# Kernel optimization log

Hardware: AMD Instinct MI355X
Metric: run time of the kernel (lower is better)

The kernel has to match this reference:

```python
import jax, jax.numpy as jnp
import numpy as np

NB, NLOC, DIN, DOUT = 4, 4096, 512, 512
NTYPES, TEBD = 128, 128
N_EXPERTS, TOP_K = 8, 2  # share_expert = 0 -> routed_experts = 8, routed_top_k = 2


def setup_inputs() -> dict:
    key = jax.random.key(0)
    k = jax.random.split(key, 6)
    return {
        "x": jax.random.normal(k[0], (NB, NLOC, DIN), dtype=jnp.float32),
        "type_embeddings": jax.random.normal(k[1], (NTYPES, TEBD), dtype=jnp.float32),
        "atom_types": jax.random.randint(k[2], (NB, NLOC), 0, NTYPES, dtype=jnp.int32),
        "Wg": jax.random.normal(k[3], (TEBD, N_EXPERTS), dtype=jnp.float32) / np.sqrt(TEBD),
        "We": jax.random.normal(k[4], (N_EXPERTS, DIN, DOUT), dtype=jnp.float32) / np.sqrt(DIN),
        "be": jax.random.normal(k[5], (N_EXPERTS, DOUT), dtype=jnp.float32) * 0.01,
    }


def reference(x, type_embeddings, atom_types, Wg, We, be):
    # --- route: gate on type embeddings, then index per atom (MD-continuous) ---
    logits = type_embeddings @ Wg                       # [ntypes, E]
    top_vals, top_idx = jax.lax.top_k(logits, TOP_K)    # [ntypes, K]
    weights = jax.nn.softmax(top_vals, axis=-1)         # softmax over selected logits
    atom_w = weights[atom_types]                        # [nb, nloc, K]
    atom_i = top_idx[atom_types]                        # [nb, nloc, K]

    # scatter-add top-k weights into dense per-expert weights (matches scatter_add_)
    onehot = jax.nn.one_hot(atom_i, N_EXPERTS, dtype=x.dtype)   # [nb, nloc, K, E]
    per_expert_w = jnp.einsum("bnk,bnke->bne", atom_w, onehot)  # [nb, nloc, E]

    # --- run all experts densely (the batched JIT-friendly path), then combine ---
    expert_out = jnp.tanh(jnp.einsum("bnd,edo->bneo", x, We) + be)  # [nb, nloc, E, dout]
    out = jnp.einsum("bne,bneo->bno", per_expert_w, expert_out)     # [nb, nloc, dout]
    return out
```

## Files before the change

### kernel.cpp

```cpp
#include <hip/hip_runtime.h>
#include <hip/hip_bf16.h>
#include <math.h>

typedef __bf16 bf16;
typedef __bf16 bf16x8 __attribute__((ext_vector_type(8)));
typedef float  f32x4  __attribute__((ext_vector_type(4)));

#define NTOK   16384
#define DIN    512
#define DOUT   512
#define NTYPES 128
#define TEBD   128
#define NEXP   8
#define NPAIR  64
#define MAXTILE 192

#define WS_ROUTE_P 0
#define WS_ROUTE_W 1024
#define WS_CNT     3072
#define WS_OFF     3584
#define WS_BASE    4096
#define WS_NTILE   4608
#define WS_TMAP    5120
#define WS_RMAP    8192
#define WS_WGT     (WS_RMAP + NTOK * 4)
#define WS_XG      (WS_WGT + NTOK * 8)
#define WS_WET     (WS_XG + (size_t)NTOK * DIN * 2)

#define GLOAD_LDS16(g, l)                                                     \
  __builtin_amdgcn_global_load_lds(                                           \
      (const __attribute__((address_space(1))) void*)(g),                     \
      (__attribute__((address_space(3))) void*)(l), 16, 0, 0)

__global__ void route_kernel(const float* __restrict__ emb,
                             const float* __restrict__ Wg,
                             int* __restrict__ route_p,
                             float* __restrict__ route_w,
                             int* __restrict__ cnt,
                             int* __restrict__ off) {
  int t = threadIdx.x;
  if (t < NPAIR) { cnt[t] = 0; off[t] = 0; }
  if (t >= NTYPES) return;
  const float* er = emb + (size_t)t * TEBD;
  float lg[NEXP];
#pragma unroll
  for (int e = 0; e < NEXP; ++e) lg[e] = 0.f;
  for (int j = 0; j < TEBD; ++j) {
    float ev = er[j];
#pragma unroll
    for (int e = 0; e < NEXP; ++e) lg[e] += ev * Wg[j * NEXP + e];
  }
  float v0 = -__builtin_inff(), v1 = -__builtin_inff();
  int i0 = 0, i1 = 0;
#pragma unroll
  for (int e = 0; e < NEXP; ++e) {
    float v = lg[e];
    if (v > v0) { v1 = v0; i1 = i0; v0 = v; i0 = e; }
    else if (v > v1) { v1 = v; i1 = e; }
  }
  float d = expf(v1 - v0);
  float inv = 1.f / (1.f + d);
  route_p[t] = i0 * 8 + i1;
  route_w[t * 2 + 0] = inv;
  route_w[t * 2 + 1] = d * inv;
}

__global__ void count_kernel(const int* __restrict__ atype,
                             const int* __restrict__ route_p,
                             int* __restrict__ cnt) {
  __shared__ int lc[NPAIR];
  int tid = threadIdx.x;
  if (tid < NPAIR) lc[tid] = 0;
  __syncthreads();
  int t = blockIdx.x * 256 + tid;
  int p = route_p[atype[t]];
  atomicAdd(&lc[p], 1);
  __syncthreads();
  if (tid < NPAIR && lc[tid]) atomicAdd(&cnt[tid], lc[tid]);
}

__global__ void scan_kernel(const int* __restrict__ cnt,
                            int* __restrict__ base,
                            int* __restrict__ ntile,
                            int* __restrict__ tmap) {
  __shared__ int sb[NPAIR];
  __shared__ int st[NPAIR];
  int l = threadIdx.x;
  int c = cnt[l];
  sb[l] = c;
  st[l] = (c + 127) >> 7;
  __syncthreads();
  int b = 0, tb = 0;
  for (int j = 0; j < l; ++j) { b += sb[j]; tb += st[j]; }
  base[l] = b;
  int nt_l = st[l];
  for (int i = 0; i < nt_l; ++i) {
    tmap[(tb + i) * 2 + 0] = l;
    tmap[(tb + i) * 2 + 1] = i * 128;
  }
  if (l == NPAIR - 1) ntile[0] = tb + nt_l;
}

__global__ void place_kernel(const int* __restrict__ atype,
                             const int* __restrict__ route_p,
                             const float* __restrict__ route_w,
                             const int* __restrict__ base,
                             int* __restrict__ off,
                             int* __restrict__ row_map,
                             float* __restrict__ wgt) {
  __shared__ int lc[NPAIR];
  __shared__ int lb[NPAIR];
  int tid = threadIdx.x;
  if (tid < NPAIR) lc[tid] = 0;
  __syncthreads();
  int t = blockIdx.x * 256 + tid;
  int ty = atype[t];
  int p = route_p[ty];
  int r = atomicAdd(&lc[p], 1);
  __syncthreads();
  if (tid < NPAIR) lb[tid] = lc[tid] ? atomicAdd(&off[tid], lc[tid]) : 0;
  __syncthreads();
  int pos = base[p] + lb[p] + r;
  row_map[pos] = t;
  ((float2*)wgt)[pos] = ((const float2*)route_w)[ty];
}

__global__ void gather_cvt_kernel(const float* __restrict__ x,
                                  const int* __restrict__ row_map,
                                  bf16* __restrict__ xg) {
  int gid = blockIdx.x * 256 + threadIdx.x;
  int row = gid >> 6;
  int c8 = (gid & 63) * 8;
  int tok = row_map[row];
  const float4* p = (const float4*)(x + (size_t)tok * DIN + c8);
  float4 a = p[0], b = p[1];
  bf16x8 o;
  o[0] = (bf16)a.x; o[1] = (bf16)a.y; o[2] = (bf16)a.z; o[3] = (bf16)a.w;
  o[4] = (bf16)b.x; o[5] = (bf16)b.y; o[6] = (bf16)b.z; o[7] = (bf16)b.w;
  *(bf16x8*)(xg + (size_t)row * DIN + c8) = o;
}

__global__ void cvt_weT_kernel(const float* __restrict__ We, bf16* __restrict__ WeT) {
  __shared__ float t[64][65];
  int bx = blockIdx.x;
  int e = bx >> 6;
  int rem = bx & 63;
  int kt = (rem >> 3) * 64;
  int nt = (rem & 7) * 64;
  int tid = threadIdx.x;
  int col = tid & 63;
  int rq = tid >> 6;
#pragma unroll
  for (int r = 0; r < 16; ++r) {
    int row = rq * 16 + r;
    t[row][col] = We[((size_t)e * DIN + kt + row) * DOUT + nt + col];
  }
  __syncthreads();
#pragma unroll
  for (int r = 0; r < 16; ++r) {
    int n = rq * 16 + r;
    WeT[((size_t)e * DOUT + nt + n) * DIN + kt + col] = (bf16)t[col][n];
  }
}

__global__ __launch_bounds__(256, 3) void moe_gemm_pair_kernel(
    const bf16* __restrict__ xg, const bf16* __restrict__ WeT,
    const float* __restrict__ be, const int* __restrict__ cnt,
    const int* __restrict__ base, const int* __restrict__ ntile,
    const int* __restrict__ tmap, const int* __restrict__ row_map,
    const float* __restrict__ wgt, float* __restrict__ out) {
  int nwork = ntile[0] * 8;
  int f = blockIdx.y * 8 + blockIdx.x;
  if (f >= nwork) return;
  int q = nwork >> 3, r = nwork & 7;
  int xcd = f & 7, idx = f >> 3;
  int L = (xcd < r ? xcd * (q + 1) : r * (q + 1) + (xcd - r) * q) + idx;
  int ti = L >> 3;
  int cx = L & 7;
  int list = tmap[ti * 2 + 0];
  int r0   = tmap[ti * 2 + 1];
  int e0 = list >> 3, e1 = list & 7;
  int nrow = cnt[list] - r0;
  if (nrow > 128) nrow = 128;
  int c0 = cx * 64;
  int arow0 = base[list] + r0;

  __shared__ __align__(16) bf16 As[3][128 * 32];
  __shared__ __align__(16) bf16 B0s[3][64 * 32];
  __shared__ __align__(16) bf16 B1s[3][64 * 32];
  __shared__ int   tokS[128];
  __shared__ float w0S[128], w1S[128];
  __shared__ float be0S[64], be1S[64];

  int tid = threadIdx.x;
  int lane = tid & 63, w = tid >> 6;

  if (tid < 128) {
    int srow = (tid < nrow) ? tid : (nrow - 1);
    int gl = arow0 + srow;
    tokS[tid] = row_map[gl];
    float2 ww = ((const float2*)wgt)[gl];
    w0S[tid] = ww.x;
    w1S[tid] = ww.y;
    if (tid < 64) {
      be0S[tid] = be[e0 * DOUT + c0 + tid];
      be1S[tid] = be[e1 * DOUT + c0 + tid];
    }
  }
  __syncthreads();

  const bf16* srcA[2];
#pragma unroll
  for (int j = 0; j < 2; ++j) {
    int slot = w * 128 + j * 64 + lane;
    int row = slot >> 2, cs = slot & 3;
    int c = cs ^ ((row >> 1) & 3);
    int srow = (row < nrow) ? row : (nrow - 1);
    srcA[j] = xg + (size_t)(arow0 + srow) * DIN + c * 8;
  }
  const bf16* srcB0;
  const bf16* srcB1;
  {
    int slot = w * 64 + lane;
    int row = slot >> 2, cs = slot & 3;
    int c = cs ^ ((row >> 1) & 3);
    srcB0 = WeT + ((size_t)e0 * DOUT + c0 + row) * DIN + c * 8;
    srcB1 = WeT + ((size_t)e1 * DOUT + c0 + row) * DIN + c * 8;
  }

  f32x4 acc0[4][2], acc1[4][2];
#pragma unroll
  for (int mi = 0; mi < 4; ++mi)
#pragma unroll
    for (int ni = 0; ni < 2; ++ni) { acc0[mi][ni] = (f32x4)0.f; acc1[mi][ni] = (f32x4)0.f; }

  int wm = (w >> 1) * 64;
  int wn = (w & 1) * 32;
  int r16 = lane & 15, g16 = lane >> 4;

  int offA[4], offB[2];
#pragma unroll
  for (int i = 0; i < 4; ++i) {
    int rA = wm + i * 16 + r16;
    offA[i] = rA * 32 + (g16 ^ ((rA >> 1) & 3)) * 8;
  }
#pragma unroll
  for (int i = 0; i < 2; ++i) {
    int rB = wn + i * 16 + r16;
    offB[i] = rB * 32 + (g16 ^ ((rB >> 1) & 3)) * 8;
  }

  auto stage = [&](int buf) {
#pragma unroll
    for (int j = 0; j < 2; ++j) {
      GLOAD_LDS16(srcA[j], &As[buf][(w * 128 + j * 64) * 8]);
      srcA[j] += 32;
    }
    GLOAD_LDS16(srcB0, &B0s[buf][w * 64 * 8]);
    GLOAD_LDS16(srcB1, &B1s[buf][w * 64 * 8]);
    srcB0 += 32;
    srcB1 += 32;
  };

  stage(0);
  stage(1);

#pragma unroll
  for (int t = 0; t < 16; ++t) {
    if (t < 15) asm volatile("s_waitcnt vmcnt(4)" ::: "memory");
    else        asm volatile("s_waitcnt vmcnt(0)" ::: "memory");
    __builtin_amdgcn_s_barrier();
    if (t + 2 < 16) stage((t + 2) % 3);

    int cur = t % 3;
    bf16x8 af[4], b0f[2], b1f[2];
#pragma unroll
    for (int i = 0; i < 4; ++i) af[i] = *(const bf16x8*)&As[cur][offA[i]];
#pragma unroll
    for (int i = 0; i < 2; ++i) b0f[i] = *(const bf16x8*)&B0s[cur][offB[i]];
#pragma unroll
    for (int i = 0; i < 2; ++i) b1f[i] = *(const bf16x8*)&B1s[cur][offB[i]];
    __builtin_amdgcn_s_setprio(1);
#pragma unroll
    for (int mi = 0; mi < 4; ++mi)
#pragma unroll
      for (int ni = 0; ni < 2; ++ni) {
        acc0[mi][ni] = __builtin_amdgcn_mfma_f32_16x16x32_bf16(
            af[mi], b0f[ni], acc0[mi][ni], 0, 0, 0);
        acc1[mi][ni] = __builtin_amdgcn_mfma_f32_16x16x32_bf16(
            af[mi], b1f[ni], acc1[mi][ni], 0, 0, 0);
      }
    __builtin_amdgcn_s_setprio(0);
  }

#pragma unroll
  for (int mi = 0; mi < 4; ++mi) {
#pragma unroll
    for (int ni = 0; ni < 2; ++ni) {
      f32x4 v0 = acc0[mi][ni];
      f32x4 v1 = acc1[mi][ni];
      int colLocal = wn + ni * 16 + r16;
      float bev0 = be0S[colLocal];
      float bev1 = be1S[colLocal];
#pragma unroll
      for (int r = 0; r < 4; ++r) {
        int lrow = wm + mi * 16 + g16 * 4 + r;
        if (lrow < nrow) {
          float val = tanhf(v0[r] + bev0) * w0S[lrow] +
                      tanhf(v1[r] + bev1) * w1S[lrow];
          out[(size_t)tokS[lrow] * DOUT + c0 + colLocal] = val;
        }
      }
    }
  }
}

extern "C" void kernel_launch(void* const* d_in, const int* in_sizes, int n_in,
                              void* d_out, int out_size, void* d_ws, size_t ws_size,
                              hipStream_t stream) {
  const float* x    = (const float*)d_in[0];
  const float* emb  = (const float*)d_in[1];
  const int*   aty  = (const int*)d_in[2];
  const float* Wg   = (const float*)d_in[3];
  const float* We   = (const float*)d_in[4];
  const float* be   = (const float*)d_in[5];
  float* out = (float*)d_out;

  char* ws = (char*)d_ws;
  int*   route_p  = (int*)(ws + WS_ROUTE_P);
  float* route_w  = (float*)(ws + WS_ROUTE_W);
  int*   cnt      = (int*)(ws + WS_CNT);
  int*   off      = (int*)(ws + WS_OFF);
  int*   base     = (int*)(ws + WS_BASE);
  int*   ntile    = (int*)(ws + WS_NTILE);
  int*   tmap     = (int*)(ws + WS_TMAP);
  int*   row_map  = (int*)(ws + WS_RMAP);
  float* wgt      = (float*)(ws + WS_WGT);
  bf16*  xg       = (bf16*)(ws + WS_XG);
  bf16*  WeT      = (bf16*)(ws + WS_WET);

  route_kernel<<<1, 128, 0, stream>>>(emb, Wg, route_p, route_w, cnt, off);
  count_kernel<<<NTOK / 256, 256, 0, stream>>>(aty, route_p, cnt);
  scan_kernel<<<1, 64, 0, stream>>>(cnt, base, ntile, tmap);
  place_kernel<<<NTOK / 256, 256, 0, stream>>>(aty, route_p, route_w, base, off,
                                               row_map, wgt);
  gather_cvt_kernel<<<(NTOK * 64) / 256, 256, 0, stream>>>(x, row_map, xg);
  cvt_weT_kernel<<<512, 256, 0, stream>>>(We, WeT);
  moe_gemm_pair_kernel<<<dim3(8, MAXTILE), 256, 0, stream>>>(
      xg, WeT, be, cnt, base, ntile, tmap, row_map, wgt, out);
}
```

Before: 78.99 us.

## Restructure routing into type histogram, fused scan, and merged gather/convert prep kernel

Replaces the per-pair count/scan/place pipeline with a per-type histogram followed by a single-block route+scan kernel that derives per-type base offsets. Token placement, x gather-to-bf16 and We transpose-convert are merged into one prep kernel, so fewer launches remain on the critical path and the x conversion no longer waits on a separate placement pass. The epilogue tanh is replaced by clamped exp2/rcp hardware instructions, with one shared reciprocal for both experts. This lowers launch count and transcendental cost, at the price of slightly different tanh precision and a global atomic cursor per type.

```diff
diff --git a/kernel.cpp b/kernel.cpp
--- a/kernel.cpp
+++ b/kernel.cpp
@@ -15,14 +15,15 @@
 #define NPAIR  64
 #define MAXTILE 192
 
-#define WS_ROUTE_P 0
-#define WS_ROUTE_W 1024
-#define WS_CNT     3072
-#define WS_OFF     3584
-#define WS_BASE    4096
-#define WS_NTILE   4608
-#define WS_TMAP    5120
-#define WS_RMAP    8192
+#define WS_HIST    0
+#define WS_ROUTE_W 512
+#define WS_BASET   1536
+#define WS_CURS    2048
+#define WS_CNTP    2560
+#define WS_BASEP   2816
+#define WS_NTILE   3072
+#define WS_TMAP    3584
+#define WS_RMAP    5120
 #define WS_WGT     (WS_RMAP + NTOK * 4)
 #define WS_XG      (WS_WGT + NTOK * 8)
 #define WS_WET     (WS_XG + (size_t)NTOK * DIN * 2)
@@ -32,15 +33,34 @@
       (const __attribute__((address_space(1))) void*)(g),                     \
       (__attribute__((address_space(3))) void*)(l), 16, 0, 0)
 
-__global__ void route_kernel(const float* __restrict__ emb,
-                             const float* __restrict__ Wg,
-                             int* __restrict__ route_p,
-                             float* __restrict__ route_w,
-                             int* __restrict__ cnt,
-                             int* __restrict__ off) {
+__global__ void hist_kernel(const int* __restrict__ atype, int* __restrict__ hist) {
+  __shared__ int h[NTYPES];
+  int tid = threadIdx.x;
+  if (tid < NTYPES) h[tid] = 0;
+  __syncthreads();
+  int t = blockIdx.x * 256 + tid;
+  atomicAdd(&h[atype[t]], 1);
+  __syncthreads();
+  if (tid < NTYPES && h[tid]) atomicAdd(&hist[tid], h[tid]);
+}
+
+__global__ void route_scan_kernel(const float* __restrict__ emb,
+                                  const float* __restrict__ Wg,
+                                  const int* __restrict__ hist,
+                                  float* __restrict__ route_w,
+                                  int* __restrict__ base_type,
+                                  int* __restrict__ cursor,
+                                  int* __restrict__ cnt_pair,
+                                  int* __restrict__ base_pair,
+                                  int* __restrict__ ntile,
+                                  int* __restrict__ tmap) {
+  __shared__ int s_cnt[NPAIR];
+  __shared__ int s_off[NTYPES];
+  __shared__ int s_pair[NTYPES];
   int t = threadIdx.x;
-  if (t < NPAIR) { cnt[t] = 0; off[t] = 0; }
-  if (t >= NTYPES) return;
+  if (t < NPAIR) s_cnt[t] = 0;
+  __syncthreads();
+
   const float* er = emb + (size_t)t * TEBD;
   float lg[NEXP];
 #pragma unroll
@@ -60,113 +80,92 @@
   }
   float d = expf(v1 - v0);
   float inv = 1.f / (1.f + d);
-  route_p[t] = i0 * 8 + i1;
   route_w[t * 2 + 0] = inv;
   route_w[t * 2 + 1] = d * inv;
-}
-
-__global__ void count_kernel(const int* __restrict__ atype,
-                             const int* __restrict__ route_p,
-                             int* __restrict__ cnt) {
-  __shared__ int lc[NPAIR];
+  int p = i0 * 8 + i1;
+  s_pair[t] = p;
+  s_off[t] = atomicAdd(&s_cnt[p], hist[t]);
+  cursor[t] = 0;
+  __syncthreads();
+
+  if (t < NPAIR) {
+    int b = 0, tb = 0;
+    for (int j = 0; j < t; ++j) { b += s_cnt[j]; tb += (s_cnt[j] + 127) >> 7; }
+    base_pair[t] = b;
+    cnt_pair[t] = s_cnt[t];
+    int nt_l = (s_cnt[t] + 127) >> 7;
+    for (int i = 0; i < nt_l; ++i) {
+      tmap[(tb + i) * 2 + 0] = t;
+      tmap[(tb + i) * 2 + 1] = i * 128;
+    }
+    if (t == NPAIR - 1) ntile[0] = tb + nt_l;
+  }
+  __syncthreads();
+  base_type[t] = base_pair[s_pair[t]] + s_off[t];
+}
+
+__global__ void prep_kernel(const float* __restrict__ x,
+                            const float* __restrict__ We,
+                            const int* __restrict__ atype,
+                            const float* __restrict__ route_w,
+                            const int* __restrict__ base_type,
+                            int* __restrict__ cursor,
+                            int* __restrict__ row_map,
+                            float* __restrict__ wgt,
+                            bf16* __restrict__ xg,
+                            bf16* __restrict__ WeT) {
+  int bx = blockIdx.x;
   int tid = threadIdx.x;
-  if (tid < NPAIR) lc[tid] = 0;
-  __syncthreads();
-  int t = blockIdx.x * 256 + tid;
-  int p = route_p[atype[t]];
-  atomicAdd(&lc[p], 1);
-  __syncthreads();
-  if (tid < NPAIR && lc[tid]) atomicAdd(&cnt[tid], lc[tid]);
-}
-
-__global__ void scan_kernel(const int* __restrict__ cnt,
-                            int* __restrict__ base,
-                            int* __restrict__ ntile,
-                            int* __restrict__ tmap) {
-  __shared__ int sb[NPAIR];
-  __shared__ int st[NPAIR];
-  int l = threadIdx.x;
-  int c = cnt[l];
-  sb[l] = c;
-  st[l] = (c + 127) >> 7;
-  __syncthreads();
-  int b = 0, tb = 0;
-  for (int j = 0; j < l; ++j) { b += sb[j]; tb += st[j]; }
-  base[l] = b;
-  int nt_l = st[l];
-  for (int i = 0; i < nt_l; ++i) {
-    tmap[(tb + i) * 2 + 0] = l;
-    tmap[(tb + i) * 2 + 1] = i * 128;
-  }
-  if (l == NPAIR - 1) ntile[0] = tb + nt_l;
-}
-
-__global__ void place_kernel(const int* __restrict__ atype,
-                             const int* __restrict__ route_p,
-                             const float* __restrict__ route_w,
-                             const int* __restrict__ base,
-                             int* __restrict__ off,
-                             int* __restrict__ row_map,
-                             float* __restrict__ wgt) {
-  __shared__ int lc[NPAIR];
-  __shared__ int lb[NPAIR];
-  int tid = threadIdx.x;
-  if (tid < NPAIR) lc[tid] = 0;
-  __syncthreads();
-  int t = blockIdx.x * 256 + tid;
-  int ty = atype[t];
-  int p = route_p[ty];
-  int r = atomicAdd(&lc[p], 1);
-  __syncthreads();
-  if (tid < NPAIR) lb[tid] = lc[tid] ? atomicAdd(&off[tid], lc[tid]) : 0;
-  __syncthreads();
-  int pos = base[p] + lb[p] + r;
-  row_map[pos] = t;
-  ((float2*)wgt)[pos] = ((const float2*)route_w)[ty];
-}
-
-__global__ void gather_cvt_kernel(const float* __restrict__ x,
-                                  const int* __restrict__ row_map,
-                                  bf16* __restrict__ xg) {
-  int gid = blockIdx.x * 256 + threadIdx.x;
-  int row = gid >> 6;
-  int c8 = (gid & 63) * 8;
-  int tok = row_map[row];
-  const float4* p = (const float4*)(x + (size_t)tok * DIN + c8);
-  float4 a = p[0], b = p[1];
-  bf16x8 o;
-  o[0] = (bf16)a.x; o[1] = (bf16)a.y; o[2] = (bf16)a.z; o[3] = (bf16)a.w;
-  o[4] = (bf16)b.x; o[5] = (bf16)b.y; o[6] = (bf16)b.z; o[7] = (bf16)b.w;
-  *(bf16x8*)(xg + (size_t)row * DIN + c8) = o;
-}
-
-__global__ void cvt_weT_kernel(const float* __restrict__ We, bf16* __restrict__ WeT) {
-  __shared__ float t[64][65];
-  int bx = blockIdx.x;
-  int e = bx >> 6;
-  int rem = bx & 63;
-  int kt = (rem >> 3) * 64;
-  int nt = (rem & 7) * 64;
-  int tid = threadIdx.x;
-  int col = tid & 63;
-  int rq = tid >> 6;
-#pragma unroll
-  for (int r = 0; r < 16; ++r) {
-    int row = rq * 16 + r;
-    t[row][col] = We[((size_t)e * DIN + kt + row) * DOUT + nt + col];
-  }
-  __syncthreads();
-#pragma unroll
-  for (int r = 0; r < 16; ++r) {
-    int n = rq * 16 + r;
-    WeT[((size_t)e * DOUT + nt + n) * DIN + kt + col] = (bf16)t[col][n];
+  if (bx < 256) {
+    __shared__ int posS[64];
+    int t0 = bx * 64;
+    if (tid < 64) {
+      int t = t0 + tid;
+      int ty = atype[t];
+      int pos = base_type[ty] + atomicAdd(&cursor[ty], 1);
+      posS[tid] = pos;
+      row_map[pos] = t;
+      ((float2*)wgt)[pos] = ((const float2*)route_w)[ty];
+    }
+    __syncthreads();
+    int w = tid >> 6, lane = tid & 63;
+#pragma unroll
+    for (int i = 0; i < 16; ++i) {
+      int r = w * 16 + i;
+      const float4* p = (const float4*)(x + (size_t)(t0 + r) * DIN + lane * 8);
+      float4 a = p[0], b = p[1];
+      bf16x8 o;
+      o[0] = (bf16)a.x; o[1] = (bf16)a.y; o[2] = (bf16)a.z; o[3] = (bf16)a.w;
+      o[4] = (bf16)b.x; o[5] = (bf16)b.y; o[6] = (bf16)b.z; o[7] = (bf16)b.w;
+      *(bf16x8*)(xg + (size_t)posS[r] * DIN + lane * 8) = o;
+    }
+  } else {
+    __shared__ float t[64][65];
+    int b2 = bx - 256;
+    int e = b2 >> 6;
+    int rem = b2 & 63;
+    int kt = (rem >> 3) * 64;
+    int nt = (rem & 7) * 64;
+    int col = tid & 63;
+    int rq = tid >> 6;
+#pragma unroll
+    for (int r = 0; r < 16; ++r) {
+      int row = rq * 16 + r;
+      t[row][col] = We[((size_t)e * DIN + kt + row) * DOUT + nt + col];
+    }
+    __syncthreads();
+#pragma unroll
+    for (int r = 0; r < 16; ++r) {
+      int n = rq * 16 + r;
+      WeT[((size_t)e * DOUT + nt + n) * DIN + kt + col] = (bf16)t[col][n];
+    }
   }
 }
 
 __global__ __launch_bounds__(256, 3) void moe_gemm_pair_kernel(
     const bf16* __restrict__ xg, const bf16* __restrict__ WeT,
-    const float* __restrict__ be, const int* __restrict__ cnt,
-    const int* __restrict__ base, const int* __restrict__ ntile,
+    const float* __restrict__ be, const int* __restrict__ cnt_pair,
+    const int* __restrict__ base_pair, const int* __restrict__ ntile,
     const int* __restrict__ tmap, const int* __restrict__ row_map,
     const float* __restrict__ wgt, float* __restrict__ out) {
   int nwork = ntile[0] * 8;
@@ -180,10 +179,10 @@
   int list = tmap[ti * 2 + 0];
   int r0   = tmap[ti * 2 + 1];
   int e0 = list >> 3, e1 = list & 7;
-  int nrow = cnt[list] - r0;
+  int nrow = cnt_pair[list] - r0;
   if (nrow > 128) nrow = 128;
   int c0 = cx * 64;
-  int arow0 = base[list] + r0;
+  int arow0 = base_pair[list] + r0;
 
   __shared__ __align__(16) bf16 As[3][128 * 32];
   __shared__ __align__(16) bf16 B0s[3][64 * 32];
@@ -306,9 +305,17 @@
       for (int r = 0; r < 4; ++r) {
         int lrow = wm + mi * 16 + g16 * 4 + r;
         if (lrow < nrow) {
-          float val = tanhf(v0[r] + bev0) * w0S[lrow] +
-                      tanhf(v1[r] + bev1) * w1S[lrow];
-          out[(size_t)tokS[lrow] * DOUT + c0 + colLocal] = val;
+          float x0 = fminf(9.f, fmaxf(-9.f, v0[r] + bev0)) * 2.885390082f;
+          float x1 = fminf(9.f, fmaxf(-9.f, v1[r] + bev1)) * 2.885390082f;
+          float e0v, e1v, invd;
+          asm("v_exp_f32 %0, %1" : "=v"(e0v) : "v"(x0));
+          asm("v_exp_f32 %0, %1" : "=v"(e1v) : "v"(x1));
+          float d0 = e0v + 1.f, d1 = e1v + 1.f;
+          asm("v_rcp_f32 %0, %1" : "=v"(invd) : "v"(d0 * d1));
+          float t0 = (e0v - 1.f) * d1 * invd;
+          float t1 = (e1v - 1.f) * d0 * invd;
+          out[(size_t)tokS[lrow] * DOUT + c0 + colLocal] =
+              t0 * w0S[lrow] + t1 * w1S[lrow];
         }
       }
     }
@@ -327,25 +334,25 @@
   float* out = (float*)d_out;
 
   char* ws = (char*)d_ws;
-  int*   route_p  = (int*)(ws + WS_ROUTE_P);
-  float* route_w  = (float*)(ws + WS_ROUTE_W);
-  int*   cnt      = (int*)(ws + WS_CNT);
-  int*   off      = (int*)(ws + WS_OFF);
-  int*   base     = (int*)(ws + WS_BASE);
-  int*   ntile    = (int*)(ws + WS_NTILE);
-  int*   tmap     = (int*)(ws + WS_TMAP);
-  int*   row_map  = (int*)(ws + WS_RMAP);
-  float* wgt      = (float*)(ws + WS_WGT);
-  bf16*  xg       = (bf16*)(ws + WS_XG);
-  bf16*  WeT      = (bf16*)(ws + WS_WET);
-
-  route_kernel<<<1, 128, 0, stream>>>(emb, Wg, route_p, route_w, cnt, off);
-  count_kernel<<<NTOK / 256, 256, 0, stream>>>(aty, route_p, cnt);
-  scan_kernel<<<1, 64, 0, stream>>>(cnt, base, ntile, tmap);
-  place_kernel<<<NTOK / 256, 256, 0, stream>>>(aty, route_p, route_w, base, off,
-                                               row_map, wgt);
-  gather_cvt_kernel<<<(NTOK * 64) / 256, 256, 0, stream>>>(x, row_map, xg);
-  cvt_weT_kernel<<<512, 256, 0, stream>>>(We, WeT);
+  int*   hist      = (int*)(ws + WS_HIST);
+  float* route_w   = (float*)(ws + WS_ROUTE_W);
+  int*   base_type = (int*)(ws + WS_BASET);
+  int*   cursor    = (int*)(ws + WS_CURS);
+  int*   cnt_pair  = (int*)(ws + WS_CNTP);
+  int*   base_pair = (int*)(ws + WS_BASEP);
+  int*   ntile     = (int*)(ws + WS_NTILE);
+  int*   tmap      = (int*)(ws + WS_TMAP);
+  int*   row_map   = (int*)(ws + WS_RMAP);
+  float* wgt       = (float*)(ws + WS_WGT);
+  bf16*  xg        = (bf16*)(ws + WS_XG);
+  bf16*  WeT       = (bf16*)(ws + WS_WET);
+
+  hipMemsetAsync(hist, 0, NTYPES * sizeof(int), stream);
+  hist_kernel<<<NTOK / 256, 256, 0, stream>>>(aty, hist);
+  route_scan_kernel<<<1, 128, 0, stream>>>(emb, Wg, hist, route_w, base_type,
+                                           cursor, cnt_pair, base_pair, ntile, tmap);
+  prep_kernel<<<256 + 512, 256, 0, stream>>>(x, We, aty, route_w, base_type,
+                                             cursor, row_map, wgt, xg, WeT);
   moe_gemm_pair_kernel<<<dim3(8, MAXTILE), 256, 0, stream>>>(
-      xg, WeT, be, cnt, base, ntile, tmap, row_map, wgt, out);
-}
+      xg, WeT, be, cnt_pair, base_pair, ntile, tmap, row_map, wgt, out);
+}
```

Measured after the change: 77.87 us. Within noise of the previous version (-1.4%).
